# Kernel optimization log

Measured on AMD Instinct MI355X. Metric: run time of the kernel, lower is better.

The kernel has to match this reference:

```python
import jax, jax.numpy as jnp
import numpy as np

D = 1024

def setup_inputs() -> dict:
    key = jax.random.key(0)
    ks = jax.random.split(key, 16)
    B, S = 8, 2048
    s = 1.0 / np.sqrt(D)
    inp = {
        "visual_feat": jax.random.normal(ks[0], (B, S, D), jnp.float32),
        "audio_feat": jax.random.normal(ks[1], (B, S, D), jnp.float32),
        "Wq": jax.random.normal(ks[2], (D, D), jnp.float32) * s,
        "bq": jnp.zeros((D,), jnp.float32),
        "Wk": jax.random.normal(ks[3], (D, D), jnp.float32) * s,
        "bk": jnp.zeros((D,), jnp.float32),
        "Wv": jax.random.normal(ks[4], (D, D), jnp.float32) * s,
        "bv": jnp.zeros((D,), jnp.float32),
        "Wo": jax.random.normal(ks[5], (D, D), jnp.float32) * s,
        "bo": jnp.zeros((D,), jnp.float32),
        "W1": jax.random.normal(ks[6], (D, D), jnp.float32) * s,
        "b1": jnp.zeros((D,), jnp.float32),
        "W2": jax.random.normal(ks[7], (D, 1), jnp.float32) * s,
        "b2": jnp.zeros((1,), jnp.float32),
    }
    return inp

def reference(visual_feat, audio_feat, Wq, bq, Wk, bk, Wv, bv, Wo, bo, W1, b1, W2, b2):
    # Cross-modal attention: query from visual, key/value from audio.
    q = jnp.einsum('bsd,de->bse', visual_feat, Wq) + bq
    k = jnp.einsum('bsd,de->bse', audio_feat, Wk) + bk
    v = jnp.einsum('bsd,de->bse', audio_feat, Wv) + bv
    # NOTE: original has NO 1/sqrt(d) scaling — faithful to source.
    scores = jnp.einsum('bqe,bke->bqk', q, k)          # [B, S, S]
    attn = jax.nn.softmax(scores, axis=-1)
    attended = jnp.einsum('bqk,bke->bqe', attn, v)     # [B, S, D]
    attended = jnp.einsum('bse,ef->bsf', attended, Wo) + bo
    h = attended + visual_feat                          # residual
    x = jax.nn.relu(jnp.einsum('bsd,de->bse', h, W1) + b1)
    out = jnp.einsum('bsd,do->bso', x, W2) + b2        # [B, S, 1]
    return out
```

## Files before the change

### kernel.cpp

```cpp
#include <hip/hip_runtime.h>
#include <cstdint>
#include <cstddef>

typedef _Float16 f16;
typedef _Float16 f16x8 __attribute__((ext_vector_type(8)));
typedef _Float16 f16x4 __attribute__((ext_vector_type(4)));
typedef float    f32x4 __attribute__((ext_vector_type(4)));

#define AS1 __attribute__((address_space(1)))
#define AS3 __attribute__((address_space(3)))

static constexpr int BB = 8;
static constexpr int SS = 2048;
static constexpr int DD = 1024;
static constexpr int MTOT = BB * SS;

__global__ __launch_bounds__(256) void cast_f32_f16(const float* __restrict__ src,
                                                    f16* __restrict__ dst, int n4) {
  int i = blockIdx.x * 256 + threadIdx.x;
  if (i < n4) {
    const float4 f = reinterpret_cast<const float4*>(src)[i];
    f16x4 o = { (f16)f.x, (f16)f.y, (f16)f.z, (f16)f.w };
    reinterpret_cast<f16x4*>(dst)[i] = o;
  }
}

__global__ __launch_bounds__(256) void transpose_cast_wt(const float* __restrict__ W,
                                                         f16* __restrict__ WT, int D) {
  __shared__ float tile[32][33];
  const int bx = blockIdx.x * 32;
  const int by = blockIdx.y * 32;
  const int tx = threadIdx.x & 31;
  const int ty = threadIdx.x >> 5;
  for (int i = ty; i < 32; i += 8) tile[i][tx] = W[(size_t)(by + i) * D + bx + tx];
  __syncthreads();
  for (int i = ty; i < 32; i += 8)
    WT[(size_t)(bx + i) * D + by + tx] = (f16)tile[tx][i];
}

__global__ __launch_bounds__(256) void transpose_f16_batch(const f16* __restrict__ src,
                                                           f16* __restrict__ dst,
                                                           int R, int C) {
  __shared__ f16 tile[32][33];
  src += (size_t)blockIdx.z * R * C;
  dst += (size_t)blockIdx.z * R * C;
  const int bx = blockIdx.x * 32;
  const int by = blockIdx.y * 32;
  const int tx = threadIdx.x & 31;
  const int ty = threadIdx.x >> 5;
  for (int i = ty; i < 32; i += 8) tile[i][tx] = src[(size_t)(by + i) * C + bx + tx];
  __syncthreads();
  for (int i = ty; i < 32; i += 8) dst[(size_t)(bx + i) * R + by + tx] = tile[tx][i];
}

template <int EPI>
__global__ __launch_bounds__(512, 2) void gemm8(
    const f16* __restrict__ A, const f16* __restrict__ A2, int zsplit,
    const f16* __restrict__ BT, void* __restrict__ Cout,
    const float* __restrict__ bias, const float* __restrict__ resid,
    int N, int K, int gx,
    size_t Abat, size_t Bbat, size_t Cbat) {
  __shared__ f16 smA[2][256 * 64];
  __shared__ f16 smB[2][256 * 64];

  const int bz = blockIdx.z;
  const f16* Ab = (zsplit && bz >= zsplit) ? A2 + (size_t)(bz - zsplit) * Abat
                                           : A + (size_t)bz * Abat;
  BT += (size_t)bz * Bbat;

  const int nwg = gridDim.x;
  const int q = nwg >> 3, r = nwg & 7;
  const int xcd = blockIdx.x & 7, lin = blockIdx.x >> 3;
  const int wg = (xcd < r ? xcd * (q + 1) : r * (q + 1) + (xcd - r) * q) + lin;
  const int n0 = (wg % gx) * 256;
  const int m0 = (wg / gx) * 256;

  const int tid = threadIdx.x;
  const int w = tid >> 6, lane = tid & 63;
  const int wr = w >> 2, wc = w & 3;
  const int lg = lane >> 4, lr = lane & 15;
  const int nt = K >> 6;

  f32x4 acc[8][4] = {};
  f16x8 alo[4][2], ahi[4][2], bfr[2][2];

  auto stageA = [&](int t, int h, int d) {
#pragma unroll
    for (int l = 0; l < 2; ++l) {
      const int cb = l * 512 + w * 64;
      const int c = cb + lane;
      const int rr = c >> 3;
      const int g = (c & 7) ^ (rr & 7);
      const f16* src = Ab + (size_t)(m0 + h * 128 + rr) * K + t * 64 + g * 8;
      __builtin_amdgcn_global_load_lds((const AS1 void*)src,
          (AS3 void*)(&smA[d][(h * 1024 + cb) * 8]), 16, 0, 0);
    }
  };
  auto stageB = [&](int t, int h, int d) {
#pragma unroll
    for (int l = 0; l < 2; ++l) {
      const int cb = l * 512 + w * 64;
      const int c = cb + lane;
      const int rr = c >> 3;
      const int g = (c & 7) ^ (rr & 7);
      const f16* src = BT + (size_t)(n0 + h * 128 + rr) * K + t * 64 + g * 8;
      __builtin_amdgcn_global_load_lds((const AS1 void*)src,
          (AS3 void*)(&smB[d][(h * 1024 + cb) * 8]), 16, 0, 0);
    }
  };
  auto lda = [&](f16x8 (&dst)[4][2], int mh, int d) {
#pragma unroll
    for (int i = 0; i < 4; ++i) {
      const int rrow = wr * 128 + (mh * 4 + i) * 16 + lr;
#pragma unroll
      for (int kh = 0; kh < 2; ++kh) {
        const int kg = (kh * 4 + lg) ^ (rrow & 7);
        dst[i][kh] = *(const f16x8*)(&smA[d][rrow * 64 + kg * 8]);
      }
    }
  };
  auto ldb = [&](int nh, int d) {
#pragma unroll
    for (int j = 0; j < 2; ++j) {
      const int nrow = wc * 64 + (nh * 2 + j) * 16 + lr;
#pragma unroll
      for (int kh = 0; kh < 2; ++kh) {
        const int kg = (kh * 4 + lg) ^ (nrow & 7);
        bfr[j][kh] = *(const f16x8*)(&smB[d][nrow * 64 + kg * 8]);
      }
    }
  };
  auto mma = [&](const f16x8 (&a)[4][2], int mh, int nh) {
#pragma unroll
    for (int i = 0; i < 4; ++i)
#pragma unroll
      for (int j = 0; j < 2; ++j)
#pragma unroll
        for (int kh = 0; kh < 2; ++kh)
          acc[mh * 4 + i][nh * 2 + j] = __builtin_amdgcn_mfma_f32_16x16x32_f16(
              a[i][kh], bfr[j][kh], acc[mh * 4 + i][nh * 2 + j], 0, 0, 0);
  };

#define PH_MID()                                                     \
  __builtin_amdgcn_sched_barrier(0);                                 \
  __builtin_amdgcn_s_barrier();                                      \
  asm volatile("s_waitcnt lgkmcnt(0)" ::: "memory");                 \
  __builtin_amdgcn_sched_barrier(0);                                 \
  __builtin_amdgcn_s_setprio(1)
#define PH_END()                                                     \
  __builtin_amdgcn_s_setprio(0);                                     \
  __builtin_amdgcn_sched_barrier(0);                                 \
  __builtin_amdgcn_s_barrier()
#define PH_END_VM4()                                                 \
  __builtin_amdgcn_s_setprio(0);                                     \
  asm volatile("s_waitcnt vmcnt(4)" ::: "memory");                   \
  __builtin_amdgcn_sched_barrier(0);                                 \
  __builtin_amdgcn_s_barrier()
#define PH_END_VM0()                                                 \
  __builtin_amdgcn_s_setprio(0);                                     \
  asm volatile("s_waitcnt vmcnt(0)" ::: "memory");                   \
  __builtin_amdgcn_sched_barrier(0);                                 \
  __builtin_amdgcn_s_barrier()

  stageA(0, 0, 0); stageA(0, 1, 0);
  stageB(0, 0, 0); stageB(0, 1, 0);
  if (nt > 1) { stageA(1, 0, 1); stageA(1, 1, 1); }
  asm volatile("s_waitcnt vmcnt(4)" ::: "memory");
  __builtin_amdgcn_sched_barrier(0);
  __builtin_amdgcn_s_barrier();

  for (int t = 0; t < nt; t += 2) {
    const int u = t + 1;
    const bool pok = (t + 2 < nt);
    lda(alo, 0, 0); ldb(0, 0); stageB(u, 0, 1);
    PH_MID(); mma(alo, 0, 0); PH_END();
    lda(ahi, 1, 0); stageB(u, 1, 1);
    PH_MID(); mma(ahi, 1, 0); PH_END();
    ldb(1, 0); if (pok) stageA(t + 2, 0, 0);
    PH_MID(); mma(ahi, 1, 1); PH_END();
    if (pok) stageA(t + 2, 1, 0);
    PH_MID(); mma(alo, 0, 1);
    if (pok) { PH_END_VM4(); } else { PH_END_VM0(); }
    lda(alo, 0, 1); ldb(0, 1); if (pok) stageB(t + 2, 0, 0);
    PH_MID(); mma(alo, 0, 0); PH_END();
    lda(ahi, 1, 1); if (pok) stageB(t + 2, 1, 0);
    PH_MID(); mma(ahi, 1, 0); PH_END();
    ldb(1, 1); if (pok) stageA(t + 3, 0, 1);
    PH_MID(); mma(ahi, 1, 1); PH_END();
    if (pok) stageA(t + 3, 1, 1);
    PH_MID(); mma(alo, 0, 1);
    if (pok) { PH_END_VM4(); } else { PH_END(); }
  }
#undef PH_MID
#undef PH_END
#undef PH_END_VM4
#undef PH_END_VM0

  if (EPI == 4) {
    float* part = (float*)Cout;
    const int cq = (n0 >> 6) + wc;
#pragma unroll
    for (int I = 0; I < 8; ++I) {
#pragma unroll
      for (int rr = 0; rr < 4; ++rr) {
        const int row = m0 + wr * 128 + I * 16 + lg * 4 + rr;
        float s = 0.f;
#pragma unroll
        for (int J = 0; J < 4; ++J) {
          const int col = n0 + wc * 64 + J * 16 + lr;
          float v = acc[I][J][rr] + bias[col];
          v = fmaxf(v, 0.f);
          s += v * resid[col];
        }
#pragma unroll
        for (int o = 1; o < 16; o <<= 1) s += __shfl_xor(s, o);
        if (lr == 0) part[(size_t)cq * MTOT + row] = s;
      }
    }
    return;
  }

#pragma unroll
  for (int I = 0; I < 8; ++I) {
    const int row = m0 + wr * 128 + I * 16 + lg * 4;
#pragma unroll
    for (int J = 0; J < 4; ++J) {
      const int col = n0 + wc * 64 + J * 16 + lr;
      float bval = 0.f;
      if (EPI == 0 || EPI == 3) bval = bias[col];
#pragma unroll
      for (int rr = 0; rr < 4; ++rr) {
        float v = acc[I][J][rr] + bval;
        const size_t idx = (size_t)(row + rr) * N + col;
        if (EPI == 3) v += resid[idx];
        if (EPI == 1)
          ((float*)Cout)[(size_t)bz * Cbat + idx] = v;
        else
          ((f16*)Cout)[(size_t)bz * Cbat + idx] = (f16)v;
      }
    }
  }
}

__global__ __launch_bounds__(256) void softmax_rows(const float* __restrict__ Sc,
                                                    f16* __restrict__ P) {
  const size_t row = blockIdx.x;
  const float* x = Sc + row * SS;
  f16* p = P + row * SS;
  const int t = threadIdx.x;
  const int wid = t >> 6, lane = t & 63;
  __shared__ float red[8];

  float v[8];
  float mx = -3.4e38f;
#pragma unroll
  for (int i = 0; i < 8; ++i) {
    v[i] = x[t + i * 256];
    mx = fmaxf(mx, v[i]);
  }
#pragma unroll
  for (int o = 32; o >= 1; o >>= 1) mx = fmaxf(mx, __shfl_xor(mx, o));
  if (lane == 0) red[wid] = mx;
  __syncthreads();
  mx = fmaxf(fmaxf(red[0], red[1]), fmaxf(red[2], red[3]));

  float sum = 0.f;
#pragma unroll
  for (int i = 0; i < 8; ++i) {
    v[i] = __expf(v[i] - mx);
    sum += v[i];
  }
#pragma unroll
  for (int o = 32; o >= 1; o >>= 1) sum += __shfl_xor(sum, o);
  if (lane == 0) red[4 + wid] = sum;
  __syncthreads();
  sum = red[4] + red[5] + red[6] + red[7];
  const float inv = 1.0f / sum;
#pragma unroll
  for (int i = 0; i < 8; ++i) p[t + i * 256] = (f16)(v[i] * inv);
}

__global__ __launch_bounds__(256) void reduce_out(const float* __restrict__ part,
                                                  const float* __restrict__ b2,
                                                  float* __restrict__ out) {
  const int i = blockIdx.x * 256 + threadIdx.x;
  float s = 0.f;
#pragma unroll
  for (int c = 0; c < 16; ++c) s += part[(size_t)c * MTOT + i];
  out[i] = s + b2[0];
}

extern "C" void kernel_launch(void* const* d_in, const int* in_sizes, int n_in,
                              void* d_out, int out_size, void* d_ws, size_t ws_size,
                              hipStream_t stream) {
  const float* vis = (const float*)d_in[0];
  const float* aud = (const float*)d_in[1];
  const float* Wq = (const float*)d_in[2];
  const float* bq = (const float*)d_in[3];
  const float* Wk = (const float*)d_in[4];
  const float* bk = (const float*)d_in[5];
  const float* Wv = (const float*)d_in[6];
  const float* bv = (const float*)d_in[7];
  const float* Wo = (const float*)d_in[8];
  const float* bo = (const float*)d_in[9];
  const float* W1 = (const float*)d_in[10];
  const float* b1 = (const float*)d_in[11];
  const float* W2 = (const float*)d_in[12];
  const float* b2 = (const float*)d_in[13];
  float* out = (float*)d_out;
  (void)in_sizes; (void)n_in; (void)out_size;

  char* ws = (char*)d_ws;
  size_t off = 0;
  auto carve = [&](size_t bytes) -> void* {
    void* p = ws + off;
    off += (bytes + 255) & ~(size_t)255;
    return p;
  };
  const size_t wtB = (size_t)DD * DD * sizeof(f16);
  const size_t bufB = (size_t)MTOT * DD * sizeof(f16);
  f16* WqT = (f16*)carve(wtB);
  f16* WkT = (f16*)carve(wtB);
  f16* WvT = (f16*)carve(wtB);
  f16* WoT = (f16*)carve(wtB);
  f16* W1T = (f16*)carve(wtB);
  f16* slot1 = (f16*)carve(bufB);
  f16* slot2 = (f16*)carve(bufB);
  f16* slot3 = (f16*)carve(bufB);
  f16* slot4 = (f16*)carve(bufB);

  const size_t rem = (ws_size > off) ? ws_size - off : 0;
  const size_t needMain = (size_t)4 * SS * SS * 4 + (size_t)4 * SS * SS * 2 + 512;

  f16* VIS16 = slot1;
  f16* AUD16 = slot2;
  f16* Q16 = slot3;
  f16* K16 = slot4;
  f16* V16 = slot1;
  f16* VT16 = slot2;
  f16* ATT16 = slot1;
  f16* P1 = slot3;
  f16* H16 = slot3;
  float* partials = (float*)slot4;

  const dim3 blk(256);
  const dim3 blk8(512);
  const int n4 = MTOT * DD / 4;

  cast_f32_f16<<<dim3((n4 + 255) / 256), blk, 0, stream>>>(vis, VIS16, n4);
  cast_f32_f16<<<dim3((n4 + 255) / 256), blk, 0, stream>>>(aud, AUD16, n4);

  transpose_cast_wt<<<dim3(DD / 32, DD / 32), blk, 0, stream>>>(Wq, WqT, DD);
  transpose_cast_wt<<<dim3(DD / 32, DD / 32), blk, 0, stream>>>(Wk, WkT, DD);
  transpose_cast_wt<<<dim3(DD / 32, DD / 32), blk, 0, stream>>>(Wv, WvT, DD);
  transpose_cast_wt<<<dim3(DD / 32, DD / 32), blk, 0, stream>>>(Wo, WoT, DD);
  transpose_cast_wt<<<dim3(DD / 32, DD / 32), blk, 0, stream>>>(W1, W1T, DD);

  gemm8<0><<<dim3(4 * 64, 1, 1), blk8, 0, stream>>>(
      VIS16, nullptr, 0, WqT, Q16, bq, nullptr, DD, DD, 4, 0, 0, 0);
  gemm8<0><<<dim3(4 * 64, 1, 1), blk8, 0, stream>>>(
      AUD16, nullptr, 0, WkT, K16, bk, nullptr, DD, DD, 4, 0, 0, 0);
  gemm8<0><<<dim3(4 * 64, 1, 1), blk8, 0, stream>>>(
      AUD16, nullptr, 0, WvT, V16, bv, nullptr, DD, DD, 4, 0, 0, 0);

  transpose_f16_batch<<<dim3(DD / 32, SS / 32, BB), blk, 0, stream>>>(V16, VT16, SS, DD);

  if (rem >= needMain) {
    float* S32 = (float*)carve((size_t)4 * SS * SS * sizeof(float));
    f16* P0 = (f16*)carve((size_t)4 * SS * SS * sizeof(f16));
    gemm8<1><<<dim3((SS / 256) * (SS / 256), 1, 4), blk8, 0, stream>>>(
        Q16, nullptr, 0, K16, S32, nullptr, nullptr,
        SS, DD, SS / 256, (size_t)SS * DD, (size_t)SS * DD, (size_t)SS * SS);
    softmax_rows<<<dim3(4 * SS), blk, 0, stream>>>(S32, P0);
    gemm8<1><<<dim3((SS / 256) * (SS / 256), 1, 4), blk8, 0, stream>>>(
        Q16 + (size_t)4 * SS * DD, nullptr, 0, K16 + (size_t)4 * SS * DD, S32,
        nullptr, nullptr, SS, DD, SS / 256,
        (size_t)SS * DD, (size_t)SS * DD, (size_t)SS * SS);
    softmax_rows<<<dim3(4 * SS), blk, 0, stream>>>(S32, P1);
    gemm8<2><<<dim3((DD / 256) * (SS / 256), 1, 8), blk8, 0, stream>>>(
        P0, P1, 4, VT16, ATT16, nullptr, nullptr,
        DD, SS, DD / 256, (size_t)SS * SS, (size_t)DD * SS, (size_t)SS * DD);
  } else {
    const int RB = 256;
    float* S32 = (float*)carve((size_t)RB * SS * sizeof(float));
    f16* Pc = (f16*)carve((size_t)RB * SS * sizeof(f16));
    for (int b = 0; b < BB; ++b) {
      for (int r0 = 0; r0 < SS; r0 += RB) {
        gemm8<1><<<dim3((SS / 256) * (RB / 256), 1, 1), blk8, 0, stream>>>(
            Q16 + ((size_t)b * SS + r0) * DD, nullptr, 0, K16 + (size_t)b * SS * DD,
            S32, nullptr, nullptr, SS, DD, SS / 256, 0, 0, 0);
        softmax_rows<<<dim3(RB), blk, 0, stream>>>(S32, Pc);
        gemm8<2><<<dim3((DD / 256) * (RB / 256), 1, 1), blk8, 0, stream>>>(
            Pc, nullptr, 0, VT16 + (size_t)b * DD * SS,
            ATT16 + ((size_t)b * SS + r0) * DD, nullptr, nullptr,
            DD, SS, DD / 256, 0, 0, 0);
      }
    }
  }

  gemm8<3><<<dim3(4 * 64, 1, 1), blk8, 0, stream>>>(
      ATT16, nullptr, 0, WoT, H16, bo, vis, DD, DD, 4, 0, 0, 0);

  gemm8<4><<<dim3(4 * 64, 1, 1), blk8, 0, stream>>>(
      H16, nullptr, 0, W1T, partials, b1, W2, DD, DD, 4, 0, 0, 0);

  reduce_out<<<dim3(MTOT / 256), blk, 0, stream>>>(partials, b2, out);
}
```

Baseline: 486.8 us.

## Switch GEMM to 32x32x16 MFMA, fuse K/V projections and launch prologue

The GEMM kernel now uses 32x32x16 MFMA tiles with 16-wide accumulators instead of 16x16x32, which cuts LDS fragment reads per MFMA. The K and V projections are merged into one GEMM with a concatenated transposed weight and per-column bias select, and the input casts and five weight transposes are each collapsed into one launch. Workspace is reshuffled so the attention output reuses the score buffer, and the GEMM gains separate leading dimensions to read the interleaved KV buffer. This trades extra accumulator register pressure and a strided K/V layout for fewer launches and better MFMA efficiency.

```diff
diff --git a/kernel.cpp b/kernel.cpp
--- a/kernel.cpp
+++ b/kernel.cpp
@@ -5,7 +5,7 @@
 typedef _Float16 f16;
 typedef _Float16 f16x8 __attribute__((ext_vector_type(8)));
 typedef _Float16 f16x4 __attribute__((ext_vector_type(4)));
-typedef float    f32x4 __attribute__((ext_vector_type(4)));
+typedef float    f32x16 __attribute__((ext_vector_type(16)));
 
 #define AS1 __attribute__((address_space(1)))
 #define AS3 __attribute__((address_space(3)))
@@ -15,40 +15,59 @@
 static constexpr int DD = 1024;
 static constexpr int MTOT = BB * SS;
 
-__global__ __launch_bounds__(256) void cast_f32_f16(const float* __restrict__ src,
-                                                    f16* __restrict__ dst, int n4) {
+__global__ __launch_bounds__(256) void cast2_f32_f16(const float* __restrict__ s1,
+                                                     const float* __restrict__ s2,
+                                                     f16* __restrict__ d1,
+                                                     f16* __restrict__ d2, int n4) {
   int i = blockIdx.x * 256 + threadIdx.x;
-  if (i < n4) {
-    const float4 f = reinterpret_cast<const float4*>(src)[i];
-    f16x4 o = { (f16)f.x, (f16)f.y, (f16)f.z, (f16)f.w };
-    reinterpret_cast<f16x4*>(dst)[i] = o;
-  }
-}
-
-__global__ __launch_bounds__(256) void transpose_cast_wt(const float* __restrict__ W,
-                                                         f16* __restrict__ WT, int D) {
+  const float* s;
+  f16* d;
+  int j;
+  if (i < n4) { s = s1; d = d1; j = i; }
+  else        { s = s2; d = d2; j = i - n4; if (j >= n4) return; }
+  const float4 f = reinterpret_cast<const float4*>(s)[j];
+  f16x4 o = { (f16)f.x, (f16)f.y, (f16)f.z, (f16)f.w };
+  reinterpret_cast<f16x4*>(d)[j] = o;
+}
+
+__global__ __launch_bounds__(256) void transpose_cast_wt5(
+    const float* __restrict__ W0, const float* __restrict__ W1,
+    const float* __restrict__ W2, const float* __restrict__ W3,
+    const float* __restrict__ W4,
+    f16* __restrict__ D0, f16* __restrict__ D1, f16* __restrict__ D2,
+    f16* __restrict__ D3, f16* __restrict__ D4) {
   __shared__ float tile[32][33];
+  const float* W;
+  f16* Dst;
+  switch (blockIdx.z) {
+    case 0: W = W0; Dst = D0; break;
+    case 1: W = W1; Dst = D1; break;
+    case 2: W = W2; Dst = D2; break;
+    case 3: W = W3; Dst = D3; break;
+    default: W = W4; Dst = D4; break;
+  }
   const int bx = blockIdx.x * 32;
   const int by = blockIdx.y * 32;
   const int tx = threadIdx.x & 31;
   const int ty = threadIdx.x >> 5;
-  for (int i = ty; i < 32; i += 8) tile[i][tx] = W[(size_t)(by + i) * D + bx + tx];
+  for (int i = ty; i < 32; i += 8) tile[i][tx] = W[(size_t)(by + i) * DD + bx + tx];
   __syncthreads();
   for (int i = ty; i < 32; i += 8)
-    WT[(size_t)(bx + i) * D + by + tx] = (f16)tile[tx][i];
+    Dst[(size_t)(bx + i) * DD + by + tx] = (f16)tile[tx][i];
 }
 
 __global__ __launch_bounds__(256) void transpose_f16_batch(const f16* __restrict__ src,
                                                            f16* __restrict__ dst,
-                                                           int R, int C) {
+                                                           int R, int C, int sStr,
+                                                           size_t sBat) {
   __shared__ f16 tile[32][33];
-  src += (size_t)blockIdx.z * R * C;
+  src += (size_t)blockIdx.z * sBat;
   dst += (size_t)blockIdx.z * R * C;
   const int bx = blockIdx.x * 32;
   const int by = blockIdx.y * 32;
   const int tx = threadIdx.x & 31;
   const int ty = threadIdx.x >> 5;
-  for (int i = ty; i < 32; i += 8) tile[i][tx] = src[(size_t)(by + i) * C + bx + tx];
+  for (int i = ty; i < 32; i += 8) tile[i][tx] = src[(size_t)(by + i) * sStr + bx + tx];
   __syncthreads();
   for (int i = ty; i < 32; i += 8) dst[(size_t)(bx + i) * R + by + tx] = tile[tx][i];
 }
@@ -58,7 +77,7 @@
     const f16* __restrict__ A, const f16* __restrict__ A2, int zsplit,
     const f16* __restrict__ BT, void* __restrict__ Cout,
     const float* __restrict__ bias, const float* __restrict__ resid,
-    int N, int K, int gx,
+    int N, int K, int ldA, int ldB, int gx,
     size_t Abat, size_t Bbat, size_t Cbat) {
   __shared__ f16 smA[2][256 * 64];
   __shared__ f16 smB[2][256 * 64];
@@ -78,11 +97,11 @@
   const int tid = threadIdx.x;
   const int w = tid >> 6, lane = tid & 63;
   const int wr = w >> 2, wc = w & 3;
-  const int lg = lane >> 4, lr = lane & 15;
+  const int l31 = lane & 31, l5 = lane >> 5;
   const int nt = K >> 6;
 
-  f32x4 acc[8][4] = {};
-  f16x8 alo[4][2], ahi[4][2], bfr[2][2];
+  f32x16 acc[4][2] = {};
+  f16x8 alo[2][4], ahi[2][4], bfr[4];
 
   auto stageA = [&](int t, int h, int d) {
 #pragma unroll
@@ -91,7 +110,7 @@
       const int c = cb + lane;
       const int rr = c >> 3;
       const int g = (c & 7) ^ (rr & 7);
-      const f16* src = Ab + (size_t)(m0 + h * 128 + rr) * K + t * 64 + g * 8;
+      const f16* src = Ab + (size_t)(m0 + h * 128 + rr) * ldA + t * 64 + g * 8;
       __builtin_amdgcn_global_load_lds((const AS1 void*)src,
           (AS3 void*)(&smA[d][(h * 1024 + cb) * 8]), 16, 0, 0);
     }
@@ -103,42 +122,37 @@
       const int c = cb + lane;
       const int rr = c >> 3;
       const int g = (c & 7) ^ (rr & 7);
-      const f16* src = BT + (size_t)(n0 + h * 128 + rr) * K + t * 64 + g * 8;
+      const f16* src = BT + (size_t)(n0 + h * 128 + rr) * ldB + t * 64 + g * 8;
       __builtin_amdgcn_global_load_lds((const AS1 void*)src,
           (AS3 void*)(&smB[d][(h * 1024 + cb) * 8]), 16, 0, 0);
     }
   };
-  auto lda = [&](f16x8 (&dst)[4][2], int mh, int d) {
-#pragma unroll
-    for (int i = 0; i < 4; ++i) {
-      const int rrow = wr * 128 + (mh * 4 + i) * 16 + lr;
-#pragma unroll
-      for (int kh = 0; kh < 2; ++kh) {
-        const int kg = (kh * 4 + lg) ^ (rrow & 7);
-        dst[i][kh] = *(const f16x8*)(&smA[d][rrow * 64 + kg * 8]);
+  auto rdA = [&](f16x8 (&dst)[2][4], int mh, int d) {
+#pragma unroll
+    for (int f = 0; f < 2; ++f) {
+      const int rrow = wr * 128 + (mh * 2 + f) * 32 + l31;
+#pragma unroll
+      for (int kk = 0; kk < 4; ++kk) {
+        const int kg = (kk * 2 + l5) ^ (rrow & 7);
+        dst[f][kk] = *(const f16x8*)(&smA[d][rrow * 64 + kg * 8]);
       }
     }
   };
-  auto ldb = [&](int nh, int d) {
-#pragma unroll
-    for (int j = 0; j < 2; ++j) {
-      const int nrow = wc * 64 + (nh * 2 + j) * 16 + lr;
-#pragma unroll
-      for (int kh = 0; kh < 2; ++kh) {
-        const int kg = (kh * 4 + lg) ^ (nrow & 7);
-        bfr[j][kh] = *(const f16x8*)(&smB[d][nrow * 64 + kg * 8]);
-      }
-    }
-  };
-  auto mma = [&](const f16x8 (&a)[4][2], int mh, int nh) {
-#pragma unroll
-    for (int i = 0; i < 4; ++i)
-#pragma unroll
-      for (int j = 0; j < 2; ++j)
-#pragma unroll
-        for (int kh = 0; kh < 2; ++kh)
-          acc[mh * 4 + i][nh * 2 + j] = __builtin_amdgcn_mfma_f32_16x16x32_f16(
-              a[i][kh], bfr[j][kh], acc[mh * 4 + i][nh * 2 + j], 0, 0, 0);
+  auto rdB = [&](int nh, int d) {
+    const int nrow = wc * 64 + nh * 32 + l31;
+#pragma unroll
+    for (int kk = 0; kk < 4; ++kk) {
+      const int kg = (kk * 2 + l5) ^ (nrow & 7);
+      bfr[kk] = *(const f16x8*)(&smB[d][nrow * 64 + kg * 8]);
+    }
+  };
+  auto mma = [&](const f16x8 (&a)[2][4], int mh, int nh) {
+#pragma unroll
+    for (int f = 0; f < 2; ++f)
+#pragma unroll
+      for (int kk = 0; kk < 4; ++kk)
+        acc[mh * 2 + f][nh] = __builtin_amdgcn_mfma_f32_32x32x16_f16(
+            a[f][kk], bfr[kk], acc[mh * 2 + f][nh], 0, 0, 0);
   };
 
 #define PH_MID()                                                     \
@@ -172,20 +186,20 @@
   for (int t = 0; t < nt; t += 2) {
     const int u = t + 1;
     const bool pok = (t + 2 < nt);
-    lda(alo, 0, 0); ldb(0, 0); stageB(u, 0, 1);
+    rdA(alo, 0, 0); rdB(0, 0); stageB(u, 0, 1);
     PH_MID(); mma(alo, 0, 0); PH_END();
-    lda(ahi, 1, 0); stageB(u, 1, 1);
+    rdA(ahi, 1, 0); stageB(u, 1, 1);
     PH_MID(); mma(ahi, 1, 0); PH_END();
-    ldb(1, 0); if (pok) stageA(t + 2, 0, 0);
+    rdB(1, 0); if (pok) stageA(t + 2, 0, 0);
     PH_MID(); mma(ahi, 1, 1); PH_END();
     if (pok) stageA(t + 2, 1, 0);
     PH_MID(); mma(alo, 0, 1);
     if (pok) { PH_END_VM4(); } else { PH_END_VM0(); }
-    lda(alo, 0, 1); ldb(0, 1); if (pok) stageB(t + 2, 0, 0);
+    rdA(alo, 0, 1); rdB(0, 1); if (pok) stageB(t + 2, 0, 0);
     PH_MID(); mma(alo, 0, 0); PH_END();
-    lda(ahi, 1, 1); if (pok) stageB(t + 2, 1, 0);
+    rdA(ahi, 1, 1); if (pok) stageB(t + 2, 1, 0);
     PH_MID(); mma(ahi, 1, 0); PH_END();
-    ldb(1, 1); if (pok) stageA(t + 3, 0, 1);
+    rdB(1, 1); if (pok) stageA(t + 3, 0, 1);
     PH_MID(); mma(ahi, 1, 1); PH_END();
     if (pok) stageA(t + 3, 1, 1);
     PH_MID(); mma(alo, 0, 1);
@@ -200,38 +214,40 @@
     float* part = (float*)Cout;
     const int cq = (n0 >> 6) + wc;
 #pragma unroll
-    for (int I = 0; I < 8; ++I) {
-#pragma unroll
-      for (int rr = 0; rr < 4; ++rr) {
-        const int row = m0 + wr * 128 + I * 16 + lg * 4 + rr;
+    for (int fi = 0; fi < 4; ++fi) {
+#pragma unroll
+      for (int rg = 0; rg < 16; ++rg) {
+        const int row = m0 + wr * 128 + fi * 32 + l5 * 4 + (rg & 3) + 8 * (rg >> 2);
         float s = 0.f;
 #pragma unroll
-        for (int J = 0; J < 4; ++J) {
-          const int col = n0 + wc * 64 + J * 16 + lr;
-          float v = acc[I][J][rr] + bias[col];
+        for (int nh = 0; nh < 2; ++nh) {
+          const int col = n0 + wc * 64 + nh * 32 + l31;
+          float v = acc[fi][nh][rg] + bias[col];
           v = fmaxf(v, 0.f);
           s += v * resid[col];
         }
 #pragma unroll
-        for (int o = 1; o < 16; o <<= 1) s += __shfl_xor(s, o);
-        if (lr == 0) part[(size_t)cq * MTOT + row] = s;
+        for (int o = 1; o < 32; o <<= 1) s += __shfl_xor(s, o);
+        if (l31 == 0) part[(size_t)cq * MTOT + row] = s;
       }
     }
     return;
   }
 
 #pragma unroll
-  for (int I = 0; I < 8; ++I) {
-    const int row = m0 + wr * 128 + I * 16 + lg * 4;
-#pragma unroll
-    for (int J = 0; J < 4; ++J) {
-      const int col = n0 + wc * 64 + J * 16 + lr;
+  for (int fi = 0; fi < 4; ++fi) {
+    const int rowb = m0 + wr * 128 + fi * 32 + l5 * 4;
+#pragma unroll
+    for (int nh = 0; nh < 2; ++nh) {
+      const int col = n0 + wc * 64 + nh * 32 + l31;
       float bval = 0.f;
-      if (EPI == 0 || EPI == 3) bval = bias[col];
-#pragma unroll
-      for (int rr = 0; rr < 4; ++rr) {
-        float v = acc[I][J][rr] + bval;
-        const size_t idx = (size_t)(row + rr) * N + col;
+      if (EPI == 0) bval = (col < DD) ? bias[col] : resid[col - DD];
+      if (EPI == 3) bval = bias[col];
+#pragma unroll
+      for (int rg = 0; rg < 16; ++rg) {
+        const int row = rowb + (rg & 3) + 8 * (rg >> 2);
+        float v = acc[fi][nh][rg] + bval;
+        const size_t idx = (size_t)row * N + col;
         if (EPI == 3) v += resid[idx];
         if (EPI == 1)
           ((float*)Cout)[(size_t)bz * Cbat + idx] = v;
@@ -320,89 +336,87 @@
   const size_t wtB = (size_t)DD * DD * sizeof(f16);
   const size_t bufB = (size_t)MTOT * DD * sizeof(f16);
   f16* WqT = (f16*)carve(wtB);
-  f16* WkT = (f16*)carve(wtB);
-  f16* WvT = (f16*)carve(wtB);
+  f16* KVT = (f16*)carve(2 * wtB);
   f16* WoT = (f16*)carve(wtB);
   f16* W1T = (f16*)carve(wtB);
   f16* slot1 = (f16*)carve(bufB);
   f16* slot2 = (f16*)carve(bufB);
   f16* slot3 = (f16*)carve(bufB);
-  f16* slot4 = (f16*)carve(bufB);
+  f16* KV16 = (f16*)carve(2 * bufB);
 
   const size_t rem = (ws_size > off) ? ws_size - off : 0;
-  const size_t needMain = (size_t)4 * SS * SS * 4 + (size_t)4 * SS * SS * 2 + 512;
+  const size_t needMain = (size_t)4 * SS * SS * sizeof(float) + 512;
 
   f16* VIS16 = slot1;
   f16* AUD16 = slot2;
   f16* Q16 = slot3;
-  f16* K16 = slot4;
-  f16* V16 = slot1;
-  f16* VT16 = slot2;
-  f16* ATT16 = slot1;
+  f16* VT16 = slot1;
+  f16* P0 = slot2;
   f16* P1 = slot3;
-  f16* H16 = slot3;
-  float* partials = (float*)slot4;
+  f16* H16 = slot1;
+  float* partials = (float*)slot2;
 
   const dim3 blk(256);
   const dim3 blk8(512);
   const int n4 = MTOT * DD / 4;
 
-  cast_f32_f16<<<dim3((n4 + 255) / 256), blk, 0, stream>>>(vis, VIS16, n4);
-  cast_f32_f16<<<dim3((n4 + 255) / 256), blk, 0, stream>>>(aud, AUD16, n4);
-
-  transpose_cast_wt<<<dim3(DD / 32, DD / 32), blk, 0, stream>>>(Wq, WqT, DD);
-  transpose_cast_wt<<<dim3(DD / 32, DD / 32), blk, 0, stream>>>(Wk, WkT, DD);
-  transpose_cast_wt<<<dim3(DD / 32, DD / 32), blk, 0, stream>>>(Wv, WvT, DD);
-  transpose_cast_wt<<<dim3(DD / 32, DD / 32), blk, 0, stream>>>(Wo, WoT, DD);
-  transpose_cast_wt<<<dim3(DD / 32, DD / 32), blk, 0, stream>>>(W1, W1T, DD);
+  cast2_f32_f16<<<dim3((2 * n4 + 255) / 256), blk, 0, stream>>>(
+      vis, aud, VIS16, AUD16, n4);
+
+  transpose_cast_wt5<<<dim3(DD / 32, DD / 32, 5), blk, 0, stream>>>(
+      Wq, Wk, Wv, Wo, W1, WqT, KVT, KVT + (size_t)DD * DD, WoT, W1T);
 
   gemm8<0><<<dim3(4 * 64, 1, 1), blk8, 0, stream>>>(
-      VIS16, nullptr, 0, WqT, Q16, bq, nullptr, DD, DD, 4, 0, 0, 0);
-  gemm8<0><<<dim3(4 * 64, 1, 1), blk8, 0, stream>>>(
-      AUD16, nullptr, 0, WkT, K16, bk, nullptr, DD, DD, 4, 0, 0, 0);
-  gemm8<0><<<dim3(4 * 64, 1, 1), blk8, 0, stream>>>(
-      AUD16, nullptr, 0, WvT, V16, bv, nullptr, DD, DD, 4, 0, 0, 0);
-
-  transpose_f16_batch<<<dim3(DD / 32, SS / 32, BB), blk, 0, stream>>>(V16, VT16, SS, DD);
+      VIS16, nullptr, 0, WqT, Q16, bq, bq, DD, DD, DD, DD, 4, 0, 0, 0);
+  gemm8<0><<<dim3(8 * 64, 1, 1), blk8, 0, stream>>>(
+      AUD16, nullptr, 0, KVT, KV16, bk, bv, 2 * DD, DD, DD, DD, 8, 0, 0, 0);
+
+  transpose_f16_batch<<<dim3(DD / 32, SS / 32, BB), blk, 0, stream>>>(
+      KV16 + DD, VT16, SS, DD, 2 * DD, (size_t)SS * 2 * DD);
 
   if (rem >= needMain) {
     float* S32 = (float*)carve((size_t)4 * SS * SS * sizeof(float));
-    f16* P0 = (f16*)carve((size_t)4 * SS * SS * sizeof(f16));
+    f16* ATT16 = (f16*)S32;
     gemm8<1><<<dim3((SS / 256) * (SS / 256), 1, 4), blk8, 0, stream>>>(
-        Q16, nullptr, 0, K16, S32, nullptr, nullptr,
-        SS, DD, SS / 256, (size_t)SS * DD, (size_t)SS * DD, (size_t)SS * SS);
+        Q16, nullptr, 0, KV16, S32, nullptr, nullptr,
+        SS, DD, DD, 2 * DD, SS / 256,
+        (size_t)SS * DD, (size_t)SS * 2 * DD, (size_t)SS * SS);
     softmax_rows<<<dim3(4 * SS), blk, 0, stream>>>(S32, P0);
     gemm8<1><<<dim3((SS / 256) * (SS / 256), 1, 4), blk8, 0, stream>>>(
-        Q16 + (size_t)4 * SS * DD, nullptr, 0, K16 + (size_t)4 * SS * DD, S32,
-        nullptr, nullptr, SS, DD, SS / 256,
-        (size_t)SS * DD, (size_t)SS * DD, (size_t)SS * SS);
+        Q16 + (size_t)4 * SS * DD, nullptr, 0, KV16 + (size_t)4 * SS * 2 * DD,
+        S32, nullptr, nullptr, SS, DD, DD, 2 * DD, SS / 256,
+        (size_t)SS * DD, (size_t)SS * 2 * DD, (size_t)SS * SS);
     softmax_rows<<<dim3(4 * SS), blk, 0, stream>>>(S32, P1);
     gemm8<2><<<dim3((DD / 256) * (SS / 256), 1, 8), blk8, 0, stream>>>(
         P0, P1, 4, VT16, ATT16, nullptr, nullptr,
-        DD, SS, DD / 256, (size_t)SS * SS, (size_t)DD * SS, (size_t)SS * DD);
+        DD, SS, SS, SS, DD / 256,
+        (size_t)SS * SS, (size_t)DD * SS, (size_t)SS * DD);
+    gemm8<3><<<dim3(4 * 64, 1, 1), blk8, 0, stream>>>(
+        ATT16, nullptr, 0, WoT, H16, bo, vis, DD, DD, DD, DD, 4, 0, 0, 0);
   } else {
     const int RB = 256;
     float* S32 = (float*)carve((size_t)RB * SS * sizeof(float));
     f16* Pc = (f16*)carve((size_t)RB * SS * sizeof(f16));
+    f16* ATT16 = Q16;
     for (int b = 0; b < BB; ++b) {
       for (int r0 = 0; r0 < SS; r0 += RB) {
         gemm8<1><<<dim3((SS / 256) * (RB / 256), 1, 1), blk8, 0, stream>>>(
-            Q16 + ((size_t)b * SS + r0) * DD, nullptr, 0, K16 + (size_t)b * SS * DD,
-            S32, nullptr, nullptr, SS, DD, SS / 256, 0, 0, 0);
+            Q16 + ((size_t)b * SS + r0) * DD, nullptr, 0,
+            KV16 + (size_t)b * SS * 2 * DD, S32, nullptr, nullptr,
+            SS, DD, DD, 2 * DD, SS / 256, 0, 0, 0);
         softmax_rows<<<dim3(RB), blk, 0, stream>>>(S32, Pc);
         gemm8<2><<<dim3((DD / 256) * (RB / 256), 1, 1), blk8, 0, stream>>>(
             Pc, nullptr, 0, VT16 + (size_t)b * DD * SS,
             ATT16 + ((size_t)b * SS + r0) * DD, nullptr, nullptr,
-            DD, SS, DD / 256, 0, 0, 0);
+            DD, SS, SS, SS, DD / 256, 0, 0, 0);
       }
     }
-  }
-
-  gemm8<3><<<dim3(4 * 64, 1, 1), blk8, 0, stream>>>(
-      ATT16, nullptr, 0, WoT, H16, bo, vis, DD, DD, 4, 0, 0, 0);
+    gemm8<3><<<dim3(4 * 64, 1, 1), blk8, 0, stream>>>(
+        ATT16, nullptr, 0, WoT, H16, bo, vis, DD, DD, DD, DD, 4, 0, 0, 0);
+  }
 
   gemm8<4><<<dim3(4 * 64, 1, 1), blk8, 0, stream>>>(
-      H16, nullptr, 0, W1T, partials, b1, W2, DD, DD, 4, 0, 0, 0);
+      H16, nullptr, 0, W1T, partials, b1, W2, DD, DD, DD, DD, 4, 0, 0, 0);
 
   reduce_out<<<dim3(MTOT / 256), blk, 0, stream>>>(partials, b2, out);
 }
```

Result: no change. 491.1 us (+0.9%).
